# Kernel tuning notes

Hardware: AMD Instinct MI355X
Metric: run time of the kernel (lower is better)

Reference implementation:

```python
import jax, jax.numpy as jnp
import numpy as np

B, S, H = 4, 2048, 1024
NH, HD = 16, 64
WIN = 64  # window_size = min(64, seq_len)
SCALE = float(np.sqrt(HD))


def setup_inputs() -> dict:
    key = jax.random.key(0)
    ks = jax.random.split(key, 10)
    w = lambda k, shp: (jax.random.normal(k, shp, jnp.float32) * 0.02)
    return {
        "x": jax.random.normal(ks[0], (B, S, H), jnp.float32),
        "attention_mask": jnp.ones((B, S), jnp.int32),
        "Wq": w(ks[1], (H, NH * HD)), "bq": jnp.zeros((NH * HD,), jnp.float32),
        "Wk": w(ks[2], (H, NH * HD)), "bk": jnp.zeros((NH * HD,), jnp.float32),
        "Wv": w(ks[3], (H, NH * HD)), "bv": jnp.zeros((NH * HD,), jnp.float32),
        "Wo": w(ks[4], (NH * HD, H)), "bo": jnp.zeros((H,), jnp.float32),
    }


def reference(x, attention_mask, Wq, bq, Wk, bk, Wv, bv, Wo, bo):
    # projections -> [B, NH, S, HD]
    def split_heads(t):
        return t.reshape(B, S, NH, HD).transpose(0, 2, 1, 3)
    q = split_heads(x @ Wq + bq)
    k = split_heads(x @ Wk + bk)
    v = split_heads(x @ Wv + bv)

    scores = jnp.einsum("bhqd,bhkd->bhqk", q, k) / SCALE  # [B,NH,S,S]

    # local banded mask: |i - j| <= window_size // 2
    idx = jnp.arange(S)
    local = jnp.abs(idx[None, :] - idx[:, None]) <= (WIN // 2)  # [S,S]
    scores = jnp.where(local[None, None, :, :], scores, -jnp.inf)

    # padding mask: [B,1,1,S]
    scores = jnp.where(attention_mask[:, None, None, :] == 0, -jnp.inf, scores)

    probs = jax.nn.softmax(scores, axis=-1)
    probs = jnp.nan_to_num(probs)  # rows that are fully masked -> 0

    out = jnp.einsum("bhqk,bhkd->bhqd", probs, v)
    out = out.transpose(0, 2, 1, 3).reshape(B, S, NH * HD)
    return out @ Wo + bo
```

## Files before the change

### kernel.cpp

```cpp
#include <hip/hip_runtime.h>
#include <stdint.h>

typedef unsigned short u16;
typedef __attribute__((ext_vector_type(8))) short short8;
typedef __attribute__((ext_vector_type(4))) float f32x4;

#define S_LEN 2048
#define HID   1024
#define QKV_LD 3072
#define M_ROWS 8192

__device__ __forceinline__ u16 f2bf(float f) {
  unsigned u = __float_as_uint(f);
  unsigned r = (u + 0x7fffu + ((u >> 16) & 1u)) >> 16;
  return (u16)r;
}

__device__ __forceinline__ void gload16(const u16* g, u16* l) {
  __builtin_amdgcn_global_load_lds(
      (const __attribute__((address_space(1))) unsigned int*)(g),
      (__attribute__((address_space(3))) unsigned int*)(l),
      16, 0, 0);
}

__device__ __forceinline__ void wgbar() {
  asm volatile("" ::: "memory");
  __builtin_amdgcn_s_barrier();
  asm volatile("" ::: "memory");
}

__global__ __launch_bounds__(256) void cvt_bias(
    const float* __restrict__ in, u16* __restrict__ out, int n,
    const float* __restrict__ bq, const float* __restrict__ bk,
    const float* __restrict__ bv, float* __restrict__ bqkv) {
  if (blockIdx.x == (unsigned)(n / (256 * 8))) {
    for (int i = threadIdx.x; i < 3072; i += 256)
      bqkv[i] = (i < 1024) ? bq[i] : (i < 2048) ? bk[i - 1024] : bv[i - 2048];
    return;
  }
  int i = (blockIdx.x * 256 + threadIdx.x) * 8;
  float4 a = *(const float4*)(in + i);
  float4 b = *(const float4*)(in + i + 4);
  u16 t[8];
  t[0] = f2bf(a.x); t[1] = f2bf(a.y); t[2] = f2bf(a.z); t[3] = f2bf(a.w);
  t[4] = f2bf(b.x); t[5] = f2bf(b.y); t[6] = f2bf(b.z); t[7] = f2bf(b.w);
  *(short8*)(out + i) = *(short8*)t;
}

__global__ __launch_bounds__(256) void pack_weights(
    const float* __restrict__ Wq, const float* __restrict__ Wk,
    const float* __restrict__ Wv, const float* __restrict__ Wo,
    u16* __restrict__ wqkvt, u16* __restrict__ wot) {
  __shared__ float tile[32][33];
  const int z = blockIdx.z;
  const float* in = (z == 0) ? Wq : (z == 1) ? Wk : (z == 2) ? Wv : Wo;
  u16* out = (z < 3) ? (wqkvt + (size_t)z * 1024 * 1024) : wot;
  int tx = threadIdx.x & 31, ty = threadIdx.x >> 5;
  int n0 = blockIdx.x * 32, k0 = blockIdx.y * 32;
#pragma unroll
  for (int i = 0; i < 32; i += 8)
    tile[ty + i][tx] = in[(size_t)(k0 + ty + i) * 1024 + n0 + tx];
  __syncthreads();
#pragma unroll
  for (int i = 0; i < 32; i += 8)
    out[(size_t)(n0 + ty + i) * 1024 + k0 + tx] = f2bf(tile[tx][ty + i]);
}

__global__ __launch_bounds__(256, 2) void gemm_k1(
    const u16* __restrict__ A, const u16* __restrict__ Bt,
    const float* __restrict__ bias, u16* __restrict__ C, int N) {
  constexpr int K = 1024, NT = 16;
  constexpr int BM = 128, BN = 192;
  constexpr int AU = BM * 64;
  constexpr int BUF = (BM + BN) * 64;
  __shared__ __align__(16) u16 smem[2 * BUF];

  const int tid = threadIdx.x;
  const int wave = tid >> 6, lane = tid & 63;
  const int qlane = lane & 15, kgrp = lane >> 4;
  const int wm = wave >> 1, wn = wave & 1;
  const int nbn = N / BN;
  int wg = blockIdx.x;
  const int cpx = (int)gridDim.x >> 3;
  wg = (wg & 7) * cpx + (wg >> 3);
  const int bm = wg / nbn, bn = wg % nbn;

  const int srow = tid >> 3;
  const int sslot = tid & 7;
  uint32_t gA[4], gB[6];
#pragma unroll
  for (int au = 0; au < 4; ++au) {
    int row = au * 32 + srow;
    gA[au] = (uint32_t)((bm * BM + row) * K + ((sslot ^ (row & 7)) * 8));
  }
#pragma unroll
  for (int bu = 0; bu < 6; ++bu) {
    int row = bu * 32 + srow;
    gB[bu] = (uint32_t)((bn * BN + row) * K + ((sslot ^ (row & 7)) * 8));
  }

  auto stgA = [&](int t, int au) {
    gload16(A + (size_t)gA[au] + t * 64, &smem[(t & 1) * BUF + au * 2048 + tid * 8]);
  };
  auto stgB = [&](int t, int bu) {
    gload16(Bt + (size_t)gB[bu] + t * 64, &smem[(t & 1) * BUF + AU + bu * 2048 + tid * 8]);
  };

#pragma unroll
  for (int au = 0; au < 4; ++au) stgA(0, au);
#pragma unroll
  for (int bu = 0; bu < 6; ++bu) stgB(0, bu);
#pragma unroll
  for (int au = 0; au < 4; ++au) stgA(1, au);
  stgB(1, 0); stgB(1, 1);
  asm volatile("s_waitcnt vmcnt(6)" ::: "memory");
  wgbar();

  f32x4 acc[4][6] = {};
  short8 af[4][2], bf[2][2];

  for (int t = 0; t < NT; ++t) {
    const u16* bp = &smem[(t & 1) * BUF];

#pragma unroll
    for (int mf = 0; mf < 4; ++mf)
#pragma unroll
      for (int kk = 0; kk < 2; ++kk) {
        int r = wm * 64 + mf * 16 + qlane;
        af[mf][kk] = *(const short8*)&bp[r * 64 + ((kk * 4 + kgrp) ^ (r & 7)) * 8];
      }
#pragma unroll
    for (int nf = 0; nf < 2; ++nf)
#pragma unroll
      for (int kk = 0; kk < 2; ++kk) {
        int r = wn * 96 + nf * 16 + qlane;
        bf[nf][kk] = *(const short8*)&bp[AU + r * 64 + ((kk * 4 + kgrp) ^ (r & 7)) * 8];
      }
    if (t + 1 < NT) { stgB(t + 1, 2); stgB(t + 1, 3); stgB(t + 1, 4); stgB(t + 1, 5); }
    wgbar();
    asm volatile("s_waitcnt lgkmcnt(0)" ::: "memory");
    __builtin_amdgcn_s_setprio(1);
#pragma unroll
    for (int mf = 0; mf < 4; ++mf)
#pragma unroll
      for (int nf = 0; nf < 2; ++nf)
#pragma unroll
        for (int kk = 0; kk < 2; ++kk)
          acc[mf][nf] = __builtin_amdgcn_mfma_f32_16x16x32_bf16(
              af[mf][kk], bf[nf][kk], acc[mf][nf], 0, 0, 0);
    __builtin_amdgcn_s_setprio(0);
    wgbar();

#pragma unroll
    for (int nf = 0; nf < 2; ++nf)
#pragma unroll
      for (int kk = 0; kk < 2; ++kk) {
        int r = wn * 96 + (nf + 2) * 16 + qlane;
        bf[nf][kk] = *(const short8*)&bp[AU + r * 64 + ((kk * 4 + kgrp) ^ (r & 7)) * 8];
      }
    if (t + 2 < NT) { stgA(t + 2, 0); stgA(t + 2, 1); stgA(t + 2, 2); stgA(t + 2, 3); }
    wgbar();
    asm volatile("s_waitcnt lgkmcnt(0)" ::: "memory");
    __builtin_amdgcn_s_setprio(1);
#pragma unroll
    for (int mf = 0; mf < 4; ++mf)
#pragma unroll
      for (int nf = 0; nf < 2; ++nf)
#pragma unroll
        for (int kk = 0; kk < 2; ++kk)
          acc[mf][nf + 2] = __builtin_amdgcn_mfma_f32_16x16x32_bf16(
              af[mf][kk], bf[nf][kk], acc[mf][nf + 2], 0, 0, 0);
    __builtin_amdgcn_s_setprio(0);
    wgbar();

#pragma unroll
    for (int nf = 0; nf < 2; ++nf)
#pragma unroll
      for (int kk = 0; kk < 2; ++kk) {
        int r = wn * 96 + (nf + 4) * 16 + qlane;
        bf[nf][kk] = *(const short8*)&bp[AU + r * 64 + ((kk * 4 + kgrp) ^ (r & 7)) * 8];
      }
    if (t + 2 < NT) { stgB(t + 2, 0); stgB(t + 2, 1); }
    wgbar();
    asm volatile("s_waitcnt lgkmcnt(0)" ::: "memory");
    __builtin_amdgcn_s_setprio(1);
#pragma unroll
    for (int mf = 0; mf < 4; ++mf)
#pragma unroll
      for (int nf = 0; nf < 2; ++nf)
#pragma unroll
        for (int kk = 0; kk < 2; ++kk)
          acc[mf][nf + 4] = __builtin_amdgcn_mfma_f32_16x16x32_bf16(
              af[mf][kk], bf[nf][kk], acc[mf][nf + 4], 0, 0, 0);
    __builtin_amdgcn_s_setprio(0);
    if (t + 2 < NT)      asm volatile("s_waitcnt vmcnt(6)" ::: "memory");
    else if (t + 1 < NT) asm volatile("s_waitcnt vmcnt(0)" ::: "memory");
    if (t + 1 < NT) wgbar();
  }

#pragma unroll
  for (int nf = 0; nf < 6; ++nf) {
    int col = bn * BN + wn * 96 + nf * 16 + qlane;
    float bv = bias[col];
#pragma unroll
    for (int mf = 0; mf < 4; ++mf) {
      int row0 = bm * BM + wm * 64 + mf * 16 + kgrp * 4;
#pragma unroll
      for (int r = 0; r < 4; ++r)
        C[(size_t)(row0 + r) * N + col] = f2bf(acc[mf][nf][r] + bv);
    }
  }
}

template<int OUT_BF16>
__global__ __launch_bounds__(256, 2) void gemm_bt(
    const u16* __restrict__ A, const u16* __restrict__ Bt,
    const float* __restrict__ bias, void* __restrict__ Cout,
    int M, int N, int K) {
  __shared__ __align__(16) u16 Al[128 * 64];
  __shared__ __align__(16) u16 Bl[128 * 64];
  const int tid = threadIdx.x;
  const int wave = tid >> 6, lane = tid & 63;
  const int nbn = N >> 7;
  int wg = blockIdx.x;
  const int cpx = (int)gridDim.x >> 3;
  wg = (wg & 7) * cpx + (wg >> 3);
  const int bm = wg / nbn, bn = wg % nbn;

  const int wm = wave >> 1, wn = wave & 1;
  const int lrow = lane >> 3;
  const int lslot = lane & 7;
  const int gslot = lslot ^ lrow;
  const int qlane = lane & 15, kgrp = lane >> 4;

  size_t a_off[4], b_off[4];
  u16 *al_base[4], *bl_base[4];
#pragma unroll
  for (int t = 0; t < 4; ++t) {
    int rr = (wave * 4 + t) * 8 + lrow;
    a_off[t] = (size_t)(bm * 128 + rr) * K + gslot * 8;
    b_off[t] = (size_t)(bn * 128 + rr) * K + gslot * 8;
    al_base[t] = Al + (wave * 4 + t) * 512;
    bl_base[t] = Bl + (wave * 4 + t) * 512;
  }

  f32x4 acc[4][4] = {};
  for (int kt = 0; kt < K; kt += 64) {
#pragma unroll
    for (int t = 0; t < 4; ++t) {
      gload16(A + a_off[t] + kt, al_base[t]);
      gload16(Bt + b_off[t] + kt, bl_base[t]);
    }
    __syncthreads();
#pragma unroll
    for (int kk = 0; kk < 2; ++kk) {
      short8 af[4], bf[4];
#pragma unroll
      for (int mf = 0; mf < 4; ++mf) {
        int row = wm * 64 + mf * 16 + qlane;
        int s = (kk * 4 + kgrp) ^ (row & 7);
        af[mf] = *(const short8*)&Al[row * 64 + s * 8];
      }
#pragma unroll
      for (int nf = 0; nf < 4; ++nf) {
        int row = wn * 64 + nf * 16 + qlane;
        int s = (kk * 4 + kgrp) ^ (row & 7);
        bf[nf] = *(const short8*)&Bl[row * 64 + s * 8];
      }
#pragma unroll
      for (int mf = 0; mf < 4; ++mf)
#pragma unroll
        for (int nf = 0; nf < 4; ++nf)
          acc[mf][nf] = __builtin_amdgcn_mfma_f32_16x16x32_bf16(
              af[mf], bf[nf], acc[mf][nf], 0, 0, 0);
    }
    __syncthreads();
  }

#pragma unroll
  for (int nf = 0; nf < 4; ++nf) {
    int col = bn * 128 + wn * 64 + nf * 16 + qlane;
    float bv = bias[col];
#pragma unroll
    for (int mf = 0; mf < 4; ++mf) {
      int row0 = bm * 128 + wm * 64 + mf * 16 + kgrp * 4;
#pragma unroll
      for (int r = 0; r < 4; ++r) {
        float v = acc[mf][nf][r] + bv;
        if (OUT_BF16)
          ((u16*)Cout)[(size_t)(row0 + r) * N + col] = f2bf(v);
        else
          ((float*)Cout)[(size_t)(row0 + r) * N + col] = v;
      }
    }
  }
}

__global__ __launch_bounds__(256, 2) void attn_local(
    const u16* __restrict__ qkv, const int* __restrict__ amask,
    u16* __restrict__ aout) {
  __shared__ __align__(16) u16 Kl[192][72];
  __shared__ __align__(16) u16 Vt[64][200];
  __shared__ __align__(16) u16 Pl[4][32][104];

  const int tid = threadIdx.x, wave = tid >> 6, lane = tid & 63;
  const int qlane = lane & 15, kgrp = lane >> 4;
  const int bz = blockIdx.x;
  const int qt = bz & 15, h = (bz >> 4) & 15, b = bz >> 8;
  const int qs0 = qt * 128;
  const int jt = qs0 - 32;
  const size_t rbase = (size_t)b * S_LEN;

  {
    const int r0 = tid >> 3, c0 = (tid & 7) * 8;
#pragma unroll
    for (int p = 0; p < 6; ++p) {
      int row = p * 32 + r0;
      int j = jt + row;
      u16 kv[8], vv[8];
      if (j >= 0 && j < S_LEN) {
        const u16* kp = qkv + (rbase + j) * QKV_LD + HID + h * 64 + c0;
        *(short8*)kv = *(const short8*)kp;
        *(short8*)vv = *(const short8*)(kp + HID);
      } else {
#pragma unroll
        for (int q = 0; q < 8; ++q) { kv[q] = 0; vv[q] = 0; }
      }
      *(short8*)&Kl[row][c0] = *(short8*)kv;
#pragma unroll
      for (int q = 0; q < 8; ++q) Vt[c0 + q][row] = vv[q];
    }
  }

  short8 qf[2][2];
#pragma unroll
  for (int mf = 0; mf < 2; ++mf)
#pragma unroll
    for (int kk = 0; kk < 2; ++kk)
      qf[mf][kk] = *(const short8*)(qkv +
          (rbase + qs0 + wave * 32 + mf * 16 + qlane) * QKV_LD +
          h * 64 + kk * 32 + kgrp * 8);

  __syncthreads();

  f32x4 sc[2][6] = {};
#pragma unroll
  for (int kk = 0; kk < 2; ++kk) {
    short8 kf[6];
#pragma unroll
    for (int nf = 0; nf < 6; ++nf)
      kf[nf] = *(const short8*)&Kl[wave * 32 + nf * 16 + qlane][kk * 32 + kgrp * 8];
#pragma unroll
    for (int mf = 0; mf < 2; ++mf)
#pragma unroll
      for (int nf = 0; nf < 6; ++nf)
        sc[mf][nf] = __builtin_amdgcn_mfma_f32_16x16x32_bf16(
            qf[mf][kk], kf[nf], sc[mf][nf], 0, 0, 0);
  }

  int jcol[6], mv[6];
#pragma unroll
  for (int nf = 0; nf < 6; ++nf) {
    int j = jt + wave * 32 + nf * 16 + qlane;
    jcol[nf] = j;
    mv[nf] = (j >= 0 && j < S_LEN) ? amask[rbase + j] : 0;
  }

  float inv[2][4];
#pragma unroll
  for (int mf = 0; mf < 2; ++mf) {
    const int irow0 = qs0 + wave * 32 + mf * 16 + kgrp * 4;
    float mx[4] = {-1e30f, -1e30f, -1e30f, -1e30f};
#pragma unroll
    for (int r = 0; r < 4; ++r) {
      int i = irow0 + r;
#pragma unroll
      for (int nf = 0; nf < 6; ++nf) {
        int d = i - jcol[nf];
        if (mv[nf] && d >= -32 && d <= 32) mx[r] = fmaxf(mx[r], sc[mf][nf][r]);
      }
    }
#pragma unroll
    for (int m = 1; m < 16; m <<= 1)
#pragma unroll
      for (int r = 0; r < 4; ++r)
        mx[r] = fmaxf(mx[r], __shfl_xor(mx[r], m));
    float sm[4] = {0.f, 0.f, 0.f, 0.f};
#pragma unroll
    for (int r = 0; r < 4; ++r) {
      int i = irow0 + r;
#pragma unroll
      for (int nf = 0; nf < 6; ++nf) {
        int d = i - jcol[nf];
        bool val = mv[nf] && d >= -32 && d <= 32;
        float p = val ? __expf((sc[mf][nf][r] - mx[r]) * 0.125f) : 0.f;
        sc[mf][nf][r] = p;
        sm[r] += p;
      }
    }
#pragma unroll
    for (int m = 1; m < 16; m <<= 1)
#pragma unroll
      for (int r = 0; r < 4; ++r)
        sm[r] += __shfl_xor(sm[r], m);
#pragma unroll
    for (int r = 0; r < 4; ++r)
      inv[mf][r] = sm[r] > 0.f ? 1.f / sm[r] : 0.f;
#pragma unroll
    for (int nf = 0; nf < 6; ++nf)
#pragma unroll
      for (int r = 0; r < 4; ++r)
        Pl[wave][mf * 16 + kgrp * 4 + r][nf * 16 + qlane] = f2bf(sc[mf][nf][r]);
  }
  __syncthreads();

  f32x4 oc[2][4] = {};
#pragma unroll
  for (int ks = 0; ks < 3; ++ks) {
    short8 pa[2], vb[4];
#pragma unroll
    for (int mf = 0; mf < 2; ++mf)
      pa[mf] = *(const short8*)&Pl[wave][mf * 16 + qlane][ks * 32 + kgrp * 8];
#pragma unroll
    for (int nf = 0; nf < 4; ++nf)
      vb[nf] = *(const short8*)&Vt[nf * 16 + qlane][wave * 32 + ks * 32 + kgrp * 8];
#pragma unroll
    for (int mf = 0; mf < 2; ++mf)
#pragma unroll
      for (int nf = 0; nf < 4; ++nf)
        oc[mf][nf] = __builtin_amdgcn_mfma_f32_16x16x32_bf16(
            pa[mf], vb[nf], oc[mf][nf], 0, 0, 0);
  }

#pragma unroll
  for (int mf = 0; mf < 2; ++mf)
#pragma unroll
    for (int nf = 0; nf < 4; ++nf)
#pragma unroll
      for (int r = 0; r < 4; ++r) {
        size_t row = rbase + qs0 + wave * 32 + mf * 16 + kgrp * 4 + r;
        aout[row * HID + h * 64 + nf * 16 + qlane] =
            f2bf(oc[mf][nf][r] * inv[mf][r]);
      }
}

extern "C" void kernel_launch(void* const* d_in, const int* in_sizes, int n_in,
                              void* d_out, int out_size, void* d_ws, size_t ws_size,
                              hipStream_t stream) {
  const float* x  = (const float*)d_in[0];
  const int* amask = (const int*)d_in[1];
  const float* Wq = (const float*)d_in[2];
  const float* bq = (const float*)d_in[3];
  const float* Wk = (const float*)d_in[4];
  const float* bk = (const float*)d_in[5];
  const float* Wv = (const float*)d_in[6];
  const float* bv = (const float*)d_in[7];
  const float* Wo = (const float*)d_in[8];
  const float* bo = (const float*)d_in[9];
  float* out = (float*)d_out;

  char* w = (char*)d_ws;
  u16* xb    = (u16*)w;   w += (size_t)M_ROWS * HID * 2;
  u16* wqkvt = (u16*)w;   w += (size_t)3072 * 1024 * 2;
  u16* wot   = (u16*)w;   w += (size_t)1024 * 1024 * 2;
  float* bqkv = (float*)w; w += 3072 * 4 + 256;
  u16* qkv   = (u16*)w;   w += (size_t)M_ROWS * 3072 * 2;
  u16* aout  = (u16*)w;   w += (size_t)M_ROWS * HID * 2;

  cvt_bias<<<4097, 256, 0, stream>>>(x, xb, M_ROWS * HID, bq, bk, bv, bqkv);
  pack_weights<<<dim3(32, 32, 4), 256, 0, stream>>>(Wq, Wk, Wv, Wo, wqkvt, wot);

  gemm_k1<<<1024, 256, 0, stream>>>(xb, wqkvt, bqkv, qkv, 3072);
  attn_local<<<1024, 256, 0, stream>>>(qkv, amask, aout);
  gemm_bt<0><<<64 * 8, 256, 0, stream>>>(aout, wot, bo, out, M_ROWS, 1024, 1024);
}
```

Baseline: 120.8 us.

## Merge prep kernels, pipeline output GEMM, restructure QKV GEMM phases

Folds the x conversion, bias packing and weight transpose into one launch, which saves a kernel launch and its tail. The simple single-buffered output projection GEMM is replaced by a double-buffered version that uses direct-to-LDS loads and the same phased prefetch schedule as the QKV GEMM. The QKV GEMM now runs two MFMA phases instead of three, with precomputed LDS addresses, so there are fewer barriers per K step. The cost is more register pressure from the wider B fragment arrays, plus more intricate vmcnt accounting that has to match the new load grouping.

New measurement: 115.3 us. -4.6%, faster.

```diff
diff --git a/kernel.cpp b/kernel.cpp
--- a/kernel.cpp
+++ b/kernel.cpp
@@ -29,34 +29,36 @@
   asm volatile("" ::: "memory");
 }
 
-__global__ __launch_bounds__(256) void cvt_bias(
-    const float* __restrict__ in, u16* __restrict__ out, int n,
+__global__ __launch_bounds__(256) void prep(
+    const float* __restrict__ x, u16* __restrict__ xb,
     const float* __restrict__ bq, const float* __restrict__ bk,
-    const float* __restrict__ bv, float* __restrict__ bqkv) {
-  if (blockIdx.x == (unsigned)(n / (256 * 8))) {
-    for (int i = threadIdx.x; i < 3072; i += 256)
-      bqkv[i] = (i < 1024) ? bq[i] : (i < 2048) ? bk[i - 1024] : bv[i - 2048];
-    return;
-  }
-  int i = (blockIdx.x * 256 + threadIdx.x) * 8;
-  float4 a = *(const float4*)(in + i);
-  float4 b = *(const float4*)(in + i + 4);
-  u16 t[8];
-  t[0] = f2bf(a.x); t[1] = f2bf(a.y); t[2] = f2bf(a.z); t[3] = f2bf(a.w);
-  t[4] = f2bf(b.x); t[5] = f2bf(b.y); t[6] = f2bf(b.z); t[7] = f2bf(b.w);
-  *(short8*)(out + i) = *(short8*)t;
-}
-
-__global__ __launch_bounds__(256) void pack_weights(
+    const float* __restrict__ bv, float* __restrict__ bqkv,
     const float* __restrict__ Wq, const float* __restrict__ Wk,
     const float* __restrict__ Wv, const float* __restrict__ Wo,
     u16* __restrict__ wqkvt, u16* __restrict__ wot) {
   __shared__ float tile[32][33];
-  const int z = blockIdx.z;
+  const int bid = blockIdx.x;
+  if (bid < 4096) {
+    int i = (bid * 256 + threadIdx.x) * 8;
+    float4 a = *(const float4*)(x + i);
+    float4 b = *(const float4*)(x + i + 4);
+    u16 t[8];
+    t[0] = f2bf(a.x); t[1] = f2bf(a.y); t[2] = f2bf(a.z); t[3] = f2bf(a.w);
+    t[4] = f2bf(b.x); t[5] = f2bf(b.y); t[6] = f2bf(b.z); t[7] = f2bf(b.w);
+    *(short8*)(xb + i) = *(short8*)t;
+    return;
+  }
+  if (bid == 4096) {
+    for (int i = threadIdx.x; i < 3072; i += 256)
+      bqkv[i] = (i < 1024) ? bq[i] : (i < 2048) ? bk[i - 1024] : bv[i - 2048];
+    return;
+  }
+  const int wid = bid - 4097;
+  const int z = wid >> 10, rem = wid & 1023;
   const float* in = (z == 0) ? Wq : (z == 1) ? Wk : (z == 2) ? Wv : Wo;
   u16* out = (z < 3) ? (wqkvt + (size_t)z * 1024 * 1024) : wot;
   int tx = threadIdx.x & 31, ty = threadIdx.x >> 5;
-  int n0 = blockIdx.x * 32, k0 = blockIdx.y * 32;
+  int n0 = (rem & 31) * 32, k0 = (rem >> 5) * 32;
 #pragma unroll
   for (int i = 0; i < 32; i += 8)
     tile[ty + i][tx] = in[(size_t)(k0 + ty + i) * 1024 + n0 + tx];
@@ -68,82 +70,85 @@
 
 __global__ __launch_bounds__(256, 2) void gemm_k1(
     const u16* __restrict__ A, const u16* __restrict__ Bt,
-    const float* __restrict__ bias, u16* __restrict__ C, int N) {
-  constexpr int K = 1024, NT = 16;
-  constexpr int BM = 128, BN = 192;
-  constexpr int AU = BM * 64;
-  constexpr int BUF = (BM + BN) * 64;
-  __shared__ __align__(16) u16 smem[2 * BUF];
+    const float* __restrict__ bias, u16* __restrict__ C) {
+  constexpr int K = 1024, NT = 16, N = 3072;
+  constexpr int AU = 128 * 64;
+  constexpr int SLAB = 320 * 64;
+  __shared__ __align__(16) u16 smem[2 * SLAB];
 
   const int tid = threadIdx.x;
   const int wave = tid >> 6, lane = tid & 63;
   const int qlane = lane & 15, kgrp = lane >> 4;
   const int wm = wave >> 1, wn = wave & 1;
-  const int nbn = N / BN;
   int wg = blockIdx.x;
-  const int cpx = (int)gridDim.x >> 3;
-  wg = (wg & 7) * cpx + (wg >> 3);
-  const int bm = wg / nbn, bn = wg % nbn;
+  wg = (wg & 7) * 128 + (wg >> 3);
+  const int bm = wg >> 4, bn = wg & 15;
 
   const int srow = tid >> 3;
-  const int sslot = tid & 7;
+  const int sslot = (tid & 7) ^ (srow & 7);
   uint32_t gA[4], gB[6];
 #pragma unroll
-  for (int au = 0; au < 4; ++au) {
-    int row = au * 32 + srow;
-    gA[au] = (uint32_t)((bm * BM + row) * K + ((sslot ^ (row & 7)) * 8));
-  }
-#pragma unroll
-  for (int bu = 0; bu < 6; ++bu) {
-    int row = bu * 32 + srow;
-    gB[bu] = (uint32_t)((bn * BN + row) * K + ((sslot ^ (row & 7)) * 8));
-  }
-
-  auto stgA = [&](int t, int au) {
-    gload16(A + (size_t)gA[au] + t * 64, &smem[(t & 1) * BUF + au * 2048 + tid * 8]);
+  for (int u = 0; u < 4; ++u)
+    gA[u] = (uint32_t)((bm * 128 + u * 32 + srow) * K + sslot * 8);
+#pragma unroll
+  for (int u = 0; u < 6; ++u)
+    gB[u] = (uint32_t)((bn * 192 + u * 32 + srow) * K + sslot * 8);
+
+  auto stgA = [&](int t, int u) {
+    gload16(A + (size_t)gA[u] + t * 64, &smem[(t & 1) * SLAB + u * 2048 + tid * 8]);
   };
-  auto stgB = [&](int t, int bu) {
-    gload16(Bt + (size_t)gB[bu] + t * 64, &smem[(t & 1) * BUF + AU + bu * 2048 + tid * 8]);
+  auto stgB = [&](int t, int u) {
+    gload16(Bt + (size_t)gB[u] + t * 64, &smem[(t & 1) * SLAB + AU + u * 2048 + tid * 8]);
   };
 
-#pragma unroll
-  for (int au = 0; au < 4; ++au) stgA(0, au);
-#pragma unroll
-  for (int bu = 0; bu < 6; ++bu) stgB(0, bu);
-#pragma unroll
-  for (int au = 0; au < 4; ++au) stgA(1, au);
-  stgB(1, 0); stgB(1, 1);
-  asm volatile("s_waitcnt vmcnt(6)" ::: "memory");
+  int aaddr[4], baddr[6];
+#pragma unroll
+  for (int mf = 0; mf < 4; ++mf) {
+    int r = wm * 64 + mf * 16 + qlane;
+    aaddr[mf] = r * 64;
+  }
+#pragma unroll
+  for (int nf = 0; nf < 6; ++nf) {
+    int r = wn * 96 + nf * 16 + qlane;
+    baddr[nf] = AU + r * 64;
+  }
+  const int arow7 = (wm * 64 + qlane) & 7;
+  const int brow7 = (wn * 96 + qlane) & 7;
+
+  f32x4 acc[4][6] = {};
+  short8 af[4][2], bf[4][2];
+
+#pragma unroll
+  for (int u = 0; u < 4; ++u) stgA(0, u);
+#pragma unroll
+  for (int u = 0; u < 6; ++u) stgB(0, u);
+#pragma unroll
+  for (int u = 0; u < 4; ++u) stgA(1, u);
+  stgB(1, 0); stgB(1, 1); stgB(1, 3); stgB(1, 4);
+  asm volatile("s_waitcnt vmcnt(8)" ::: "memory");
   wgbar();
 
-  f32x4 acc[4][6] = {};
-  short8 af[4][2], bf[2][2];
-
   for (int t = 0; t < NT; ++t) {
-    const u16* bp = &smem[(t & 1) * BUF];
-
-#pragma unroll
-    for (int mf = 0; mf < 4; ++mf)
-#pragma unroll
-      for (int kk = 0; kk < 2; ++kk) {
-        int r = wm * 64 + mf * 16 + qlane;
-        af[mf][kk] = *(const short8*)&bp[r * 64 + ((kk * 4 + kgrp) ^ (r & 7)) * 8];
-      }
-#pragma unroll
-    for (int nf = 0; nf < 2; ++nf)
-#pragma unroll
-      for (int kk = 0; kk < 2; ++kk) {
-        int r = wn * 96 + nf * 16 + qlane;
-        bf[nf][kk] = *(const short8*)&bp[AU + r * 64 + ((kk * 4 + kgrp) ^ (r & 7)) * 8];
-      }
-    if (t + 1 < NT) { stgB(t + 1, 2); stgB(t + 1, 3); stgB(t + 1, 4); stgB(t + 1, 5); }
+    const u16* bp = &smem[(t & 1) * SLAB];
+
+#pragma unroll
+    for (int mf = 0; mf < 4; ++mf)
+#pragma unroll
+      for (int kk = 0; kk < 2; ++kk)
+        af[mf][kk] = *(const short8*)&bp[aaddr[mf] + (((kk * 4 + kgrp) ^ arow7) * 8)];
+#pragma unroll
+    for (int nf = 0; nf < 4; ++nf)
+#pragma unroll
+      for (int kk = 0; kk < 2; ++kk)
+        bf[nf][kk] = *(const short8*)&bp[baddr[nf] + (((kk * 4 + kgrp) ^ brow7) * 8)];
+    if (t + 1 < NT) { stgB(t + 1, 2); stgB(t + 1, 5); }
     wgbar();
     asm volatile("s_waitcnt lgkmcnt(0)" ::: "memory");
     __builtin_amdgcn_s_setprio(1);
 #pragma unroll
     for (int mf = 0; mf < 4; ++mf)
 #pragma unroll
-      for (int nf = 0; nf < 2; ++nf)
+      for (int nf = 0; nf < 4; ++nf)
 #pragma unroll
         for (int kk = 0; kk < 2; ++kk)
           acc[mf][nf] = __builtin_amdgcn_mfma_f32_16x16x32_bf16(
@@ -154,11 +159,133 @@
 #pragma unroll
     for (int nf = 0; nf < 2; ++nf)
 #pragma unroll
-      for (int kk = 0; kk < 2; ++kk) {
-        int r = wn * 96 + (nf + 2) * 16 + qlane;
-        bf[nf][kk] = *(const short8*)&bp[AU + r * 64 + ((kk * 4 + kgrp) ^ (r & 7)) * 8];
-      }
-    if (t + 2 < NT) { stgA(t + 2, 0); stgA(t + 2, 1); stgA(t + 2, 2); stgA(t + 2, 3); }
+      for (int kk = 0; kk < 2; ++kk)
+        bf[nf][kk] = *(const short8*)&bp[baddr[nf + 4] + (((kk * 4 + kgrp) ^ brow7) * 8)];
+    if (t + 2 < NT) {
+      stgA(t + 2, 0); stgA(t + 2, 1); stgA(t + 2, 2); stgA(t + 2, 3);
+      stgB(t + 2, 0); stgB(t + 2, 1); stgB(t + 2, 3); stgB(t + 2, 4);
+    }
+    wgbar();
+    asm volatile("s_waitcnt lgkmcnt(0)" ::: "memory");
+    __builtin_amdgcn_s_setprio(1);
+#pragma unroll
+    for (int mf = 0; mf < 4; ++mf)
+#pragma unroll
+      for (int nf = 0; nf < 2; ++nf)
+#pragma unroll
+        for (int kk = 0; kk < 2; ++kk)
+          acc[mf][nf + 4] = __builtin_amdgcn_mfma_f32_16x16x32_bf16(
+              af[mf][kk], bf[nf][kk], acc[mf][nf + 4], 0, 0, 0);
+    __builtin_amdgcn_s_setprio(0);
+    if (t + 2 < NT)      asm volatile("s_waitcnt vmcnt(8)" ::: "memory");
+    else if (t + 1 < NT) asm volatile("s_waitcnt vmcnt(0)" ::: "memory");
+    if (t + 1 < NT) wgbar();
+  }
+
+#pragma unroll
+  for (int nf = 0; nf < 6; ++nf) {
+    int col = bn * 192 + wn * 96 + nf * 16 + qlane;
+    float bv = bias[col];
+#pragma unroll
+    for (int mf = 0; mf < 4; ++mf) {
+      int row0 = bm * 128 + wm * 64 + mf * 16 + kgrp * 4;
+#pragma unroll
+      for (int r = 0; r < 4; ++r)
+        C[(size_t)(row0 + r) * N + col] = f2bf(acc[mf][nf][r] + bv);
+    }
+  }
+}
+
+__global__ __launch_bounds__(256, 2) void gemm_k2(
+    const u16* __restrict__ A, const u16* __restrict__ Bt,
+    const float* __restrict__ bias, float* __restrict__ C) {
+  constexpr int K = 1024, NT = 16, N = 1024;
+  constexpr int AU = 128 * 64;
+  constexpr int SLAB = 256 * 64;
+  __shared__ __align__(16) u16 smem[2 * SLAB];
+
+  const int tid = threadIdx.x;
+  const int wave = tid >> 6, lane = tid & 63;
+  const int qlane = lane & 15, kgrp = lane >> 4;
+  const int wm = wave >> 1, wn = wave & 1;
+  int wg = blockIdx.x;
+  wg = (wg & 7) * 64 + (wg >> 3);
+  const int bm = wg >> 3, bn = wg & 7;
+
+  const int srow = tid >> 3;
+  const int sslot = (tid & 7) ^ (srow & 7);
+  uint32_t gA[4], gB[4];
+#pragma unroll
+  for (int u = 0; u < 4; ++u) {
+    gA[u] = (uint32_t)((bm * 128 + u * 32 + srow) * K + sslot * 8);
+    gB[u] = (uint32_t)((bn * 128 + u * 32 + srow) * K + sslot * 8);
+  }
+  auto stgA = [&](int t, int u) {
+    gload16(A + (size_t)gA[u] + t * 64, &smem[(t & 1) * SLAB + u * 2048 + tid * 8]);
+  };
+  auto stgB = [&](int t, int u) {
+    gload16(Bt + (size_t)gB[u] + t * 64, &smem[(t & 1) * SLAB + AU + u * 2048 + tid * 8]);
+  };
+
+  int aaddr[4], baddr[4];
+#pragma unroll
+  for (int f = 0; f < 4; ++f) {
+    aaddr[f] = (wm * 64 + f * 16 + qlane) * 64;
+    baddr[f] = AU + (wn * 64 + f * 16 + qlane) * 64;
+  }
+  const int arow7 = (wm * 64 + qlane) & 7;
+  const int brow7 = (wn * 64 + qlane) & 7;
+
+  f32x4 acc[4][4] = {};
+  short8 af[4][2], bf[2][2];
+
+#pragma unroll
+  for (int u = 0; u < 4; ++u) stgA(0, u);
+#pragma unroll
+  for (int u = 0; u < 4; ++u) stgB(0, u);
+#pragma unroll
+  for (int u = 0; u < 4; ++u) stgA(1, u);
+  stgB(1, 0); stgB(1, 2);
+  asm volatile("s_waitcnt vmcnt(6)" ::: "memory");
+  wgbar();
+
+  for (int t = 0; t < NT; ++t) {
+    const u16* bp = &smem[(t & 1) * SLAB];
+
+#pragma unroll
+    for (int mf = 0; mf < 4; ++mf)
+#pragma unroll
+      for (int kk = 0; kk < 2; ++kk)
+        af[mf][kk] = *(const short8*)&bp[aaddr[mf] + (((kk * 4 + kgrp) ^ arow7) * 8)];
+#pragma unroll
+    for (int nf = 0; nf < 2; ++nf)
+#pragma unroll
+      for (int kk = 0; kk < 2; ++kk)
+        bf[nf][kk] = *(const short8*)&bp[baddr[nf] + (((kk * 4 + kgrp) ^ brow7) * 8)];
+    if (t + 1 < NT) { stgB(t + 1, 1); stgB(t + 1, 3); }
+    wgbar();
+    asm volatile("s_waitcnt lgkmcnt(0)" ::: "memory");
+    __builtin_amdgcn_s_setprio(1);
+#pragma unroll
+    for (int mf = 0; mf < 4; ++mf)
+#pragma unroll
+      for (int nf = 0; nf < 2; ++nf)
+#pragma unroll
+        for (int kk = 0; kk < 2; ++kk)
+          acc[mf][nf] = __builtin_amdgcn_mfma_f32_16x16x32_bf16(
+              af[mf][kk], bf[nf][kk], acc[mf][nf], 0, 0, 0);
+    __builtin_amdgcn_s_setprio(0);
+    wgbar();
+
+#pragma unroll
+    for (int nf = 0; nf < 2; ++nf)
+#pragma unroll
+      for (int kk = 0; kk < 2; ++kk)
+        bf[nf][kk] = *(const short8*)&bp[baddr[nf + 2] + (((kk * 4 + kgrp) ^ brow7) * 8)];
+    if (t + 2 < NT) {
+      stgA(t + 2, 0); stgA(t + 2, 1); stgA(t + 2, 2); stgA(t + 2, 3);
+      stgB(t + 2, 0); stgB(t + 2, 2);
+    }
     wgbar();
     asm volatile("s_waitcnt lgkmcnt(0)" ::: "memory");
     __builtin_amdgcn_s_setprio(1);
@@ -171,113 +298,12 @@
           acc[mf][nf + 2] = __builtin_amdgcn_mfma_f32_16x16x32_bf16(
               af[mf][kk], bf[nf][kk], acc[mf][nf + 2], 0, 0, 0);
     __builtin_amdgcn_s_setprio(0);
-    wgbar();
-
-#pragma unroll
-    for (int nf = 0; nf < 2; ++nf)
-#pragma unroll
-      for (int kk = 0; kk < 2; ++kk) {
-        int r = wn * 96 + (nf + 4) * 16 + qlane;
-        bf[nf][kk] = *(const short8*)&bp[AU + r * 64 + ((kk * 4 + kgrp) ^ (r & 7)) * 8];
-      }
-    if (t + 2 < NT) { stgB(t + 2, 0); stgB(t + 2, 1); }
-    wgbar();
-    asm volatile("s_waitcnt lgkmcnt(0)" ::: "memory");
-    __builtin_amdgcn_s_setprio(1);
-#pragma unroll
-    for (int mf = 0; mf < 4; ++mf)
-#pragma unroll
-      for (int nf = 0; nf < 2; ++nf)
-#pragma unroll
-        for (int kk = 0; kk < 2; ++kk)
-          acc[mf][nf + 4] = __builtin_amdgcn_mfma_f32_16x16x32_bf16(
-              af[mf][kk], bf[nf][kk], acc[mf][nf + 4], 0, 0, 0);
-    __builtin_amdgcn_s_setprio(0);
     if (t + 2 < NT)      asm volatile("s_waitcnt vmcnt(6)" ::: "memory");
     else if (t + 1 < NT) asm volatile("s_waitcnt vmcnt(0)" ::: "memory");
     if (t + 1 < NT) wgbar();
   }
 
 #pragma unroll
-  for (int nf = 0; nf < 6; ++nf) {
-    int col = bn * BN + wn * 96 + nf * 16 + qlane;
-    float bv = bias[col];
-#pragma unroll
-    for (int mf = 0; mf < 4; ++mf) {
-      int row0 = bm * BM + wm * 64 + mf * 16 + kgrp * 4;
-#pragma unroll
-      for (int r = 0; r < 4; ++r)
-        C[(size_t)(row0 + r) * N + col] = f2bf(acc[mf][nf][r] + bv);
-    }
-  }
-}
-
-template<int OUT_BF16>
-__global__ __launch_bounds__(256, 2) void gemm_bt(
-    const u16* __restrict__ A, const u16* __restrict__ Bt,
-    const float* __restrict__ bias, void* __restrict__ Cout,
-    int M, int N, int K) {
-  __shared__ __align__(16) u16 Al[128 * 64];
-  __shared__ __align__(16) u16 Bl[128 * 64];
-  const int tid = threadIdx.x;
-  const int wave = tid >> 6, lane = tid & 63;
-  const int nbn = N >> 7;
-  int wg = blockIdx.x;
-  const int cpx = (int)gridDim.x >> 3;
-  wg = (wg & 7) * cpx + (wg >> 3);
-  const int bm = wg / nbn, bn = wg % nbn;
-
-  const int wm = wave >> 1, wn = wave & 1;
-  const int lrow = lane >> 3;
-  const int lslot = lane & 7;
-  const int gslot = lslot ^ lrow;
-  const int qlane = lane & 15, kgrp = lane >> 4;
-
-  size_t a_off[4], b_off[4];
-  u16 *al_base[4], *bl_base[4];
-#pragma unroll
-  for (int t = 0; t < 4; ++t) {
-    int rr = (wave * 4 + t) * 8 + lrow;
-    a_off[t] = (size_t)(bm * 128 + rr) * K + gslot * 8;
-    b_off[t] = (size_t)(bn * 128 + rr) * K + gslot * 8;
-    al_base[t] = Al + (wave * 4 + t) * 512;
-    bl_base[t] = Bl + (wave * 4 + t) * 512;
-  }
-
-  f32x4 acc[4][4] = {};
-  for (int kt = 0; kt < K; kt += 64) {
-#pragma unroll
-    for (int t = 0; t < 4; ++t) {
-      gload16(A + a_off[t] + kt, al_base[t]);
-      gload16(Bt + b_off[t] + kt, bl_base[t]);
-    }
-    __syncthreads();
-#pragma unroll
-    for (int kk = 0; kk < 2; ++kk) {
-      short8 af[4], bf[4];
-#pragma unroll
-      for (int mf = 0; mf < 4; ++mf) {
-        int row = wm * 64 + mf * 16 + qlane;
-        int s = (kk * 4 + kgrp) ^ (row & 7);
-        af[mf] = *(const short8*)&Al[row * 64 + s * 8];
-      }
-#pragma unroll
-      for (int nf = 0; nf < 4; ++nf) {
-        int row = wn * 64 + nf * 16 + qlane;
-        int s = (kk * 4 + kgrp) ^ (row & 7);
-        bf[nf] = *(const short8*)&Bl[row * 64 + s * 8];
-      }
-#pragma unroll
-      for (int mf = 0; mf < 4; ++mf)
-#pragma unroll
-        for (int nf = 0; nf < 4; ++nf)
-          acc[mf][nf] = __builtin_amdgcn_mfma_f32_16x16x32_bf16(
-              af[mf], bf[nf], acc[mf][nf], 0, 0, 0);
-    }
-    __syncthreads();
-  }
-
-#pragma unroll
   for (int nf = 0; nf < 4; ++nf) {
     int col = bn * 128 + wn * 64 + nf * 16 + qlane;
     float bv = bias[col];
@@ -285,13 +311,8 @@
     for (int mf = 0; mf < 4; ++mf) {
       int row0 = bm * 128 + wm * 64 + mf * 16 + kgrp * 4;
 #pragma unroll
-      for (int r = 0; r < 4; ++r) {
-        float v = acc[mf][nf][r] + bv;
-        if (OUT_BF16)
-          ((u16*)Cout)[(size_t)(row0 + r) * N + col] = f2bf(v);
-        else
-          ((float*)Cout)[(size_t)(row0 + r) * N + col] = v;
-      }
+      for (int r = 0; r < 4; ++r)
+        C[(size_t)(row0 + r) * N + col] = acc[mf][nf][r] + bv;
     }
   }
 }
@@ -467,10 +488,9 @@
   u16* qkv   = (u16*)w;   w += (size_t)M_ROWS * 3072 * 2;
   u16* aout  = (u16*)w;   w += (size_t)M_ROWS * HID * 2;
 
-  cvt_bias<<<4097, 256, 0, stream>>>(x, xb, M_ROWS * HID, bq, bk, bv, bqkv);
-  pack_weights<<<dim3(32, 32, 4), 256, 0, stream>>>(Wq, Wk, Wv, Wo, wqkvt, wot);
-
-  gemm_k1<<<1024, 256, 0, stream>>>(xb, wqkvt, bqkv, qkv, 3072);
+  prep<<<8193, 256, 0, stream>>>(x, xb, bq, bk, bv, bqkv,
+                                 Wq, Wk, Wv, Wo, wqkvt, wot);
+  gemm_k1<<<1024, 256, 0, stream>>>(xb, wqkvt, bqkv, qkv);
   attn_local<<<1024, 256, 0, stream>>>(qkv, amask, aout);
-  gemm_bt<0><<<64 * 8, 256, 0, stream>>>(aout, wot, bo, out, M_ROWS, 1024, 1024);
-}
+  gemm_k2<<<512, 256, 0, stream>>>(aout, wot, bo, out);
+}
```
